# Kernel optimization log

Measured on AMD Instinct MI355X. Metric: run time of the kernel, lower is better.

## Reference

```python
import jax, jax.numpy as jnp
import numpy as np

B, H, W, BLK = 32, 512, 512, 8
QF_MIN, QF_MAX, QF_BIAS = 2.0, 50.0, 0.0

_RGB2YCC = jnp.array([[0.299, 0.587, 0.114],
                      [-0.168736, -0.331264, 0.5],
                      [0.5, -0.418688, -0.081312]], jnp.float32)
_YCC_OFF = jnp.array([0.0, 128.0, 128.0], jnp.float32)

Y_QTB = jnp.array([16,11,10,16,24,40,51,61,12,12,14,19,26,58,60,55,14,13,16,24,40,57,69,56,
                   14,17,22,29,51,87,80,62,18,22,37,56,68,109,103,77,24,36,55,64,81,104,113,92,
                   49,64,78,87,103,121,120,101,72,92,95,98,112,100,103,99], jnp.float32).reshape(8, 8)
C_QTB = jnp.array([17,18,24,47,99,99,99,99,18,21,26,66,99,99,99,99,24,26,56,99,99,99,99,99,
                   47,66,99,99,99,99,99,99,99,99,99,99,99,99,99,99,99,99,99,99,99,99,99,99,
                   99,99,99,99,99,99,99,99,99,99,99,99,99,99,99,99], jnp.float32).reshape(8, 8)

# orthonormal 8x8 DCT-II matrix
_k = np.arange(8.0)[:, None]; _n = np.arange(8.0)[None, :]
_C = 0.5 * np.cos((2 * _n + 1) * _k * np.pi / 16.0)
_C[0] *= 1.0 / np.sqrt(2.0)
DCT_M = jnp.asarray(_C, jnp.float32)

# standard JPEG zig-zag raster order over the 64 coefficients of an 8x8 block
ZIGZAG = jnp.array([0,1,8,16,9,2,3,10,17,24,32,25,18,11,4,5,12,19,26,33,40,48,41,34,27,20,13,6,
                    7,14,21,28,35,42,49,56,57,50,43,36,29,22,15,23,30,37,44,51,58,59,52,45,38,31,
                    39,46,53,60,61,54,47,55,62,63], jnp.int32)


def hard_round(x):
    # straight-through round: forward = round(x), backward = identity
    return x + jax.lax.stop_gradient(jnp.round(x) - x)


def split_blocks(x):
    # [B,H,W] -> [B,H/8,W/8,8,8]
    b, h, w = x.shape
    return x.reshape(b, h // BLK, BLK, w // BLK, BLK).transpose(0, 1, 3, 2, 4)


def dct2d(x):
    # 2D DCT over the trailing 8x8 dims: C @ X @ C^T
    return jnp.einsum('ij,bnmjk,lk->bnmil', DCT_M, x, DCT_M)


def _norm01(e):
    mn = e.min(axis=(1, 2), keepdims=True)
    mx = e.max(axis=(1, 2), keepdims=True)
    return (e - mn) / (mx - mn + 1e-6)


def _ac_energy(d):
    # per-block log AC energy, shape [B,h8,w8]
    return jnp.log1p(jnp.sum(d * d, axis=(-2, -1)) - d[..., 0, 0] ** 2 + 1e-6)


def _forward(rgb):
    ycbcr = hard_round(jnp.einsum('bhwc,kc->bhwk', rgb, _RGB2YCC) + _YCC_OFF) - 128.0
    y_d = dct2d(split_blocks(ycbcr[..., 0]))
    cb_d = dct2d(split_blocks(ycbcr[..., 1]))
    cr_d = dct2d(split_blocks(ycbcr[..., 2]))

    # QFMapGenerator (default): per-block AC-energy rank in [0,1], upsampled to pixels
    rank = jnp.stack([_norm01(_ac_energy(y_d)),
                      _norm01(0.5 * (_ac_energy(cb_d) + _ac_energy(cr_d)))], axis=-1)  # [B,h8,w8,2]
    rank_px = jnp.repeat(jnp.repeat(rank, BLK, axis=1), BLK, axis=2)  # [B,H,W,2]

    # RankToQF
    enc_qf = jnp.clip(hard_round(QF_MIN + rank_px * (QF_MAX - QF_MIN) + QF_BIAS), QF_MIN, QF_MAX)
    y_qf_min = enc_qf[..., 0].min(axis=(1, 2), keepdims=True)
    y_qf_max = enc_qf[..., 0].max(axis=(1, 2), keepdims=True)
    c_qf_min = enc_qf[..., 1].min(axis=(1, 2), keepdims=True)
    c_qf_max = enc_qf[..., 1].max(axis=(1, 2), keepdims=True)

    # QFToScale: standard JPEG QF -> scale factor
    enc_scale = hard_round(jnp.where(enc_qf < 50.0, 5000.0 / enc_qf, 200.0 - 2.0 * enc_qf)) / 100.0

    sy = split_blocks(enc_scale[..., 0])  # [B,h8,w8,8,8]
    sc = split_blocks(enc_scale[..., 1])
    yq = hard_round(y_d / (sy * Y_QTB))
    cbq = hard_round(cb_d / (sc * C_QTB))
    crq = hard_round(cr_d / (sc * C_QTB))
    qdct = jnp.stack([yq, cbq, crq], axis=1)  # [B,3,h8,w8,8,8]

    nb = (H // BLK) * (W // BLK)
    flat = qdct.reshape(B, 3, nb, 64)
    # delta encode along the block axis
    delta = jnp.concatenate([flat[:, :, :1], flat[:, :, 1:] - flat[:, :, :-1]], axis=2)
    # zig-zag raster scan of the 64 coefficients
    zz = delta[..., ZIGZAG]
    blocks = jnp.log(jnp.abs(zz) + 1.0) / jnp.log(2.0)
    blocks = blocks.reshape(-1, 64)
    return qdct, blocks, enc_qf, enc_scale, y_qf_min, y_qf_max, c_qf_min, c_qf_max


def setup_inputs() -> dict:
    key = jax.random.key(0)
    rgb = jax.random.uniform(key, (B, H, W, 3), jnp.float32) * 255.0
    return {"rgb": rgb}


def reference(rgb):
    return _forward(rgb)
```

## Files before the change

### kernel.cpp

```cpp
#include <hip/hip_runtime.h>
#include <math.h>

#define BB 32
#define HH 512
#define WW 512
#define NB 4096
#define QD 25165824
#define PP 16777216
#define TAILOFF (2 * (size_t)QD + 2 * (size_t)PP)

constexpr int ZZc[64] = {
    0,1,8,16,9,2,3,10,17,24,32,25,18,11,4,5,12,19,26,33,40,48,41,34,27,20,13,6,
    7,14,21,28,35,42,49,56,57,50,43,36,29,22,15,23,30,37,44,51,58,59,52,45,38,31,
    39,46,53,60,61,54,47,55,62,63};
__constant__ int c_zz[64] = {
    0,1,8,16,9,2,3,10,17,24,32,25,18,11,4,5,12,19,26,33,40,48,41,34,27,20,13,6,
    7,14,21,28,35,42,49,56,57,50,43,36,29,22,15,23,30,37,44,51,58,59,52,45,38,31,
    39,46,53,60,61,54,47,55,62,63};

struct QArg { float Cf[64]; double rqY[64]; double rqC[64]; };

__device__ __forceinline__ double qf_from_rank(double r) {
    double q = rint(2.0 + r * 48.0 + 0.0);
    return fmin(fmax(q, 2.0), 50.0);
}
__device__ __forceinline__ double scale_from_qf(double qf) {
    double s = (qf < 50.0) ? (5000.0 / qf) : (200.0 - 2.0 * qf);
    return rint(s) / 100.0;
}

__device__ __forceinline__ void ycc16(const float* __restrict__ src, int p0,
                                      int* y, int* cb, int* cr) {
    float px[48];
    const float4* s4 = (const float4*)(src + (size_t)p0 * 3);
    #pragma unroll
    for (int k = 0; k < 12; ++k) ((float4*)px)[k] = s4[k];
    #pragma unroll
    for (int k = 0; k < 16; ++k) {
        double R = px[3 * k], G = px[3 * k + 1], Bv = px[3 * k + 2];
        y[k]  = (int)(rint(R * (double)0.299f     + G * (double)0.587f     + Bv * (double)0.114f)             - 128.0);
        cb[k] = (int)(rint(R * (double)-0.168736f + G * (double)-0.331264f + Bv * (double)0.5f       + 128.0) - 128.0);
        cr[k] = (int)(rint(R * (double)0.5f       + G * (double)-0.418688f + Bv * (double)-0.081312f + 128.0) - 128.0);
    }
}

__global__ __launch_bounds__(256, 4) void k_energy(const float* __restrict__ rgb,
                                                   double* __restrict__ ey,
                                                   double* __restrict__ ec) {
    __shared__ int4 part[3][8][32];
    __shared__ double ecomb[2][64];
    int b = blockIdx.x >> 6, i = blockIdx.x & 63, t = threadIdx.x;
    const float* src = rgb + (size_t)(b * HH + i * 8) * WW * 3;
    {
        int y[16], cb[16], cr[16];
        ycc16(src, t * 16, y, cb, cr);
        int s[3][2] = {{0,0},{0,0},{0,0}}, s2[3][2] = {{0,0},{0,0},{0,0}};
        #pragma unroll
        for (int k = 0; k < 16; ++k) {
            int h = k >> 3;
            s[0][h] += y[k];  s2[0][h] += y[k] * y[k];
            s[1][h] += cb[k]; s2[1][h] += cb[k] * cb[k];
            s[2][h] += cr[k]; s2[2][h] += cr[k] * cr[k];
        }
        int r0 = t >> 5, c = t & 31;
        #pragma unroll
        for (int ch = 0; ch < 3; ++ch)
            part[ch][r0][c] = make_int4(s[ch][0], s2[ch][0], s[ch][1], s2[ch][1]);
    }
    __syncthreads();
    int ch = t >> 6, j = t & 63;
    if (ch < 3) {
        int S = 0, S2 = 0;
        #pragma unroll
        for (int r = 0; r < 8; ++r) {
            const int2* p = (const int2*)&part[ch][r][j >> 1];
            int2 v = p[j & 1];
            S += v.x; S2 += v.y;
        }
        double e = log1p((double)S2 - (double)S * (double)S * (1.0 / 64.0) + 1e-6);
        if (ch == 0) ey[b * NB + i * 64 + j] = e;
        else ecomb[ch - 1][j] = e;
    }
    __syncthreads();
    if (t < 64) ec[b * NB + i * 64 + t] = 0.5 * (ecomb[0][t] + ecomb[1][t]);
}

__global__ __launch_bounds__(256) void k_minmax(const double* __restrict__ ey,
                                                const double* __restrict__ ec,
                                                double* __restrict__ mm,
                                                float* __restrict__ out_tail) {
    __shared__ double s0[256], s1[256], s2[256], s3[256];
    int b = blockIdx.x, tid = threadIdx.x;
    double mny = 1e300, mxy = -1e300, mnc = 1e300, mxc = -1e300;
    for (int n = tid; n < NB; n += 256) {
        double vy = ey[b * NB + n], vc = ec[b * NB + n];
        mny = fmin(mny, vy); mxy = fmax(mxy, vy);
        mnc = fmin(mnc, vc); mxc = fmax(mxc, vc);
    }
    s0[tid] = mny; s1[tid] = mxy; s2[tid] = mnc; s3[tid] = mxc;
    __syncthreads();
    for (int off = 128; off > 0; off >>= 1) {
        if (tid < off) {
            s0[tid] = fmin(s0[tid], s0[tid + off]);
            s1[tid] = fmax(s1[tid], s1[tid + off]);
            s2[tid] = fmin(s2[tid], s2[tid + off]);
            s3[tid] = fmax(s3[tid], s3[tid + off]);
        }
        __syncthreads();
    }
    if (tid == 0) {
        mm[b] = s0[0]; mm[32 + b] = s1[0]; mm[64 + b] = s2[0]; mm[96 + b] = s3[0];
        double ry = (s1[0] - s0[0]) / (s1[0] - s0[0] + 1e-6);
        double rc = (s3[0] - s2[0]) / (s3[0] - s2[0] + 1e-6);
        out_tail[b]      = (float)qf_from_rank(0.0);
        out_tail[32 + b] = (float)qf_from_rank(ry);
        out_tail[64 + b] = (float)qf_from_rank(0.0);
        out_tail[96 + b] = (float)qf_from_rank(rc);
    }
}

__global__ __launch_bounds__(256, 3) void k_quant(const float* __restrict__ rgb,
                                                  QArg A,
                                                  const double* __restrict__ ey,
                                                  const double* __restrict__ ec,
                                                  const double* __restrict__ mm,
                                                  float* __restrict__ out) {
    __shared__ __align__(16) char lds[53248];
    short* sqA = (short*)lds;
    short* sqB = (short*)(lds + 26112);
    float4* qsc = (float4*)(lds + 52224);
    short* planes = (short*)lds;

    int b = blockIdx.x >> 6, i = blockIdx.x & 63, t = threadIdx.x;
    {
        int y[16], cb[16], cr[16];
        ycc16(rgb + (size_t)(b * HH + i * 8) * WW * 3, t * 16, y, cb, cr);
        alignas(16) short yb[16], cbb[16], crb[16];
        #pragma unroll
        for (int k = 0; k < 16; ++k) {
            yb[k] = (short)y[k]; cbb[k] = (short)cb[k]; crb[k] = (short)cr[k];
        }
        int4* d0 = (int4*)&planes[0 * 4096 + 16 * t];
        int4* d1 = (int4*)&planes[1 * 4096 + 16 * t];
        int4* d2 = (int4*)&planes[2 * 4096 + 16 * t];
        d0[0] = ((int4*)yb)[0];  d0[1] = ((int4*)yb)[1];
        d1[0] = ((int4*)cbb)[0]; d1[1] = ((int4*)cbb)[1];
        d2[0] = ((int4*)crb)[0]; d2[1] = ((int4*)crb)[1];
    }
    __syncthreads();
    int ch = t >> 6, j = t & 63;
    float U[8][8];
    double qy = 0, qc = 0, sy = 1, sc = 1;
    if (ch < 3) {
        int gt = b * NB + i * 64 + j;
        double eyv = ey[gt], ecv = ec[gt];
        double mny = mm[b], mxy = mm[32 + b], mnc = mm[64 + b], mxc = mm[96 + b];
        double ry = (eyv - mny) / (mxy - mny + 1e-6);
        double rc = (ecv - mnc) / (mxc - mnc + 1e-6);
        qy = qf_from_rank(ry); qc = qf_from_rank(rc);
        sy = scale_from_qf(qy); sc = scale_from_qf(qc);
        #pragma unroll
        for (int r = 0; r < 8; ++r) {
            alignas(16) short xs[8];
            *(int4*)xs = *(const int4*)&planes[ch * 4096 + r * 512 + j * 8];
            float xr[8];
            #pragma unroll
            for (int s = 0; s < 8; ++s) xr[s] = (float)xs[s];
            #pragma unroll
            for (int v = 0; v < 8; ++v) {
                float u = 0.0f;
                #pragma unroll
                for (int s = 0; s < 8; ++s) u += xr[s] * A.Cf[v * 8 + s];
                U[r][v] = u;
            }
        }
    }
    __syncthreads();
    if (ch < 3) {
        if (ch == 0) qsc[j] = make_float4((float)qy, (float)qc, (float)sy, (float)sc);
        double rinv = 1.0 / ((ch == 0) ? sy : sc);
        const double* rqt = (ch == 0) ? A.rqY : A.rqC;
        int row = (ch * 64 + j) * 68;
        int qp[32];
        #pragma unroll
        for (int u = 0; u < 8; ++u) {
            alignas(8) short srow[8];
            #pragma unroll
            for (int v = 0; v < 8; ++v) {
                float dq = (float)rint([&]{
                    float d = 0.0f;
                    #pragma unroll
                    for (int r = 0; r < 8; ++r) d += A.Cf[u * 8 + r] * U[r][v];
                    return (double)d * (rqt[u * 8 + v] * rinv);
                }());
                srow[v] = (short)(int)dq;
            }
            ((long long*)&sqA[row + u * 8])[0] = ((long long*)srow)[0];
            ((long long*)&sqA[row + u * 8 + 4])[0] = ((long long*)srow)[1];
            #pragma unroll
            for (int h = 0; h < 4; ++h)
                qp[u * 4 + h] = ((int)srow[2 * h] & 0xffff) |
                                ((int)((unsigned)(int)srow[2 * h + 1] << 16));
        }
        int pp[32];
        #pragma unroll
        for (int w = 0; w < 32; ++w) pp[w] = __shfl_up(qp[w], 1, 64);
        #pragma unroll
        for (int g = 0; g < 8; ++g) {
            alignas(8) short dz[8];
            #pragma unroll
            for (int e = 0; e < 8; ++e) {
                int m = ZZc[g * 8 + e];
                int w = m >> 1;
                int cu = (m & 1) ? (qp[w] >> 16) : ((qp[w] << 16) >> 16);
                int pv = (m & 1) ? (pp[w] >> 16) : ((pp[w] << 16) >> 16);
                dz[e] = (short)(cu - pv);
            }
            ((long long*)&sqB[row + g * 8])[0] = ((long long*)dz)[0];
            ((long long*)&sqB[row + g * 8 + 4])[0] = ((long long*)dz)[1];
        }
    }
    __syncthreads();

    size_t obase = ((size_t)b * 3 * NB + (size_t)i * 64) * 64;
    #pragma unroll
    for (int it = 0; it < 12; ++it) {
        int m = it * 256 + t;
        int mch = m >> 10, f = m & 1023;
        int mj = f >> 4, k4 = (f & 15) * 4;
        alignas(8) short s4[4];
        *(long long*)s4 = *(const long long*)&sqA[(mch * 64 + mj) * 68 + k4];
        float4 v = make_float4((float)s4[0], (float)s4[1], (float)s4[2], (float)s4[3]);
        *(float4*)(out + obase + (size_t)mch * NB * 64 + (size_t)mj * 64 + k4) = v;
    }
    #pragma unroll
    for (int it = 0; it < 12; ++it) {
        int m = it * 256 + t;
        int mch = m >> 10, f = m & 1023;
        int mj = f >> 4, k4 = (f & 15) * 4;
        alignas(8) short d4[4];
        *(long long*)d4 = *(const long long*)&sqB[(mch * 64 + mj) * 68 + k4];
        float4 v = make_float4(log2f(fabsf((float)d4[0]) + 1.0f),
                               log2f(fabsf((float)d4[1]) + 1.0f),
                               log2f(fabsf((float)d4[2]) + 1.0f),
                               log2f(fabsf((float)d4[3]) + 1.0f));
        *(float4*)(out + QD + obase + (size_t)mch * NB * 64 + (size_t)mj * 64 + k4) = v;
    }
    {
        float4 qs = qsc[t >> 2];
        float4 qv = make_float4(qs.x, qs.y, qs.x, qs.y);
        float4 sv = make_float4(qs.z, qs.w, qs.z, qs.w);
        float2* mq = (float2*)(out + 2 * (size_t)QD);
        float2* ms = (float2*)(out + 2 * (size_t)QD + PP);
        #pragma unroll
        for (int rr = 0; rr < 8; ++rr) {
            size_t P = ((size_t)(b * HH + i * 8 + rr)) * WW;
            ((float4*)(mq + P))[t] = qv;
            ((float4*)(ms + P))[t] = sv;
        }
    }
}

__global__ __launch_bounds__(256) void k_fix(const float* __restrict__ q,
                                             float* __restrict__ ob) {
    int idx = blockIdx.x * 256 + threadIdx.x;
    int rid = idx >> 6, k = idx & 63;
    int bch = rid >> 6;
    int i = rid & 63;
    size_t base = ((size_t)bch * NB + (size_t)i * 64) * 64;
    int zk = c_zz[k];
    float cur = q[base + zk];
    float prv = (i > 0) ? q[base - 64 + zk] : 0.0f;
    ob[base + k] = log2f(fabsf(cur - prv) + 1.0f);
}

extern "C" void kernel_launch(void* const* d_in, const int* in_sizes, int n_in,
                              void* d_out, int out_size, void* d_ws, size_t ws_size,
                              hipStream_t stream) {
    const float* rgb = (const float*)d_in[0];
    float* out = (float*)d_out;
    double* ws = (double*)d_ws;
    double* ey = ws;
    double* ec = ws + (size_t)BB * NB;
    double* mm = ws + 2 * (size_t)BB * NB;

    static const double YQ[64] = {
        16,11,10,16,24,40,51,61, 12,12,14,19,26,58,60,55, 14,13,16,24,40,57,69,56,
        14,17,22,29,51,87,80,62, 18,22,37,56,68,109,103,77, 24,36,55,64,81,104,113,92,
        49,64,78,87,103,121,120,101, 72,92,95,98,112,100,103,99};
    static const double CQ[64] = {
        17,18,24,47,99,99,99,99, 18,21,26,66,99,99,99,99, 24,26,56,99,99,99,99,99,
        47,66,99,99,99,99,99,99, 99,99,99,99,99,99,99,99, 99,99,99,99,99,99,99,99,
        99,99,99,99,99,99,99,99, 99,99,99,99,99,99,99,99};

    QArg qa;
    for (int k = 0; k < 8; ++k)
        for (int n = 0; n < 8; ++n) {
            double v = 0.5 * cos((2.0 * n + 1.0) * (double)k * M_PI / 16.0);
            if (k == 0) v *= 0.70710678118654752440;
            qa.Cf[k * 8 + n] = (float)v;
        }
    for (int k = 0; k < 64; ++k) { qa.rqY[k] = 1.0 / YQ[k]; qa.rqC[k] = 1.0 / CQ[k]; }

    dim3 blk(256);
    k_energy<<<BB * 64, blk, 0, stream>>>(rgb, ey, ec);
    k_minmax<<<BB, blk, 0, stream>>>(ey, ec, mm, out + TAILOFF);
    k_quant<<<BB * 64, blk, 0, stream>>>(rgb, qa, ey, ec, mm, out);
    k_fix<<<(BB * 3 * 64 * 64) / 256, blk, 0, stream>>>(out, out + QD);
}
```

Before: 430.7 us.

## Cache YCbCr planes as int16 in workspace and compute delta-zigzag from LDS

k_energy now writes the rounded YCbCr values as int16 planes to workspace, and k_quant reads them back instead of reloading the float RGB input and redoing the colour conversion. The delta/zigzag stage no longer packs values and uses cross-lane shuffles into a second LDS buffer. It reads the quantized coefficients of the current and previous block straight from sqA. Dropping the rgb reload (about 3x fewer bytes) and the second LDS buffer shrinks LDS, so occupancy is raised to 4 blocks per CU. The cost is an extra global int16 write and read of about 50 MB per call.

```diff
diff --git a/kernel.cpp b/kernel.cpp
--- a/kernel.cpp
+++ b/kernel.cpp
@@ -9,10 +9,6 @@
 #define PP 16777216
 #define TAILOFF (2 * (size_t)QD + 2 * (size_t)PP)
 
-constexpr int ZZc[64] = {
-    0,1,8,16,9,2,3,10,17,24,32,25,18,11,4,5,12,19,26,33,40,48,41,34,27,20,13,6,
-    7,14,21,28,35,42,49,56,57,50,43,36,29,22,15,23,30,37,44,51,58,59,52,45,38,31,
-    39,46,53,60,61,54,47,55,62,63};
 __constant__ int c_zz[64] = {
     0,1,8,16,9,2,3,10,17,24,32,25,18,11,4,5,12,19,26,33,40,48,41,34,27,20,13,6,
     7,14,21,28,35,42,49,56,57,50,43,36,29,22,15,23,30,37,44,51,58,59,52,45,38,31,
@@ -45,6 +41,7 @@
 }
 
 __global__ __launch_bounds__(256, 4) void k_energy(const float* __restrict__ rgb,
+                                                   short* __restrict__ planes,
                                                    double* __restrict__ ey,
                                                    double* __restrict__ ec) {
     __shared__ int4 part[3][8][32];
@@ -55,13 +52,22 @@
         int y[16], cb[16], cr[16];
         ycc16(src, t * 16, y, cb, cr);
         int s[3][2] = {{0,0},{0,0},{0,0}}, s2[3][2] = {{0,0},{0,0},{0,0}};
+        alignas(16) short yb[16], cbb[16], crb[16];
         #pragma unroll
         for (int k = 0; k < 16; ++k) {
             int h = k >> 3;
             s[0][h] += y[k];  s2[0][h] += y[k] * y[k];
             s[1][h] += cb[k]; s2[1][h] += cb[k] * cb[k];
             s[2][h] += cr[k]; s2[2][h] += cr[k] * cr[k];
-        }
+            yb[k] = (short)y[k]; cbb[k] = (short)cb[k]; crb[k] = (short)cr[k];
+        }
+        size_t soff = (size_t)i * 4096 + (size_t)t * 16;
+        short* d0 = planes + (((size_t)(b * 3 + 0)) << 18) + soff;
+        short* d1 = planes + (((size_t)(b * 3 + 1)) << 18) + soff;
+        short* d2 = planes + (((size_t)(b * 3 + 2)) << 18) + soff;
+        ((int4*)d0)[0] = ((int4*)yb)[0];  ((int4*)d0)[1] = ((int4*)yb)[1];
+        ((int4*)d1)[0] = ((int4*)cbb)[0]; ((int4*)d1)[1] = ((int4*)cbb)[1];
+        ((int4*)d2)[0] = ((int4*)crb)[0]; ((int4*)d2)[1] = ((int4*)crb)[1];
         int r0 = t >> 5, c = t & 31;
         #pragma unroll
         for (int ch = 0; ch < 3; ++ch)
@@ -119,35 +125,17 @@
     }
 }
 
-__global__ __launch_bounds__(256, 3) void k_quant(const float* __restrict__ rgb,
+__global__ __launch_bounds__(256, 4) void k_quant(const short* __restrict__ planes,
                                                   QArg A,
                                                   const double* __restrict__ ey,
                                                   const double* __restrict__ ec,
                                                   const double* __restrict__ mm,
                                                   float* __restrict__ out) {
-    __shared__ __align__(16) char lds[53248];
+    __shared__ __align__(16) char lds[27136];
     short* sqA = (short*)lds;
-    short* sqB = (short*)(lds + 26112);
-    float4* qsc = (float4*)(lds + 52224);
-    short* planes = (short*)lds;
+    float4* qsc = (float4*)(lds + 26112);
 
     int b = blockIdx.x >> 6, i = blockIdx.x & 63, t = threadIdx.x;
-    {
-        int y[16], cb[16], cr[16];
-        ycc16(rgb + (size_t)(b * HH + i * 8) * WW * 3, t * 16, y, cb, cr);
-        alignas(16) short yb[16], cbb[16], crb[16];
-        #pragma unroll
-        for (int k = 0; k < 16; ++k) {
-            yb[k] = (short)y[k]; cbb[k] = (short)cb[k]; crb[k] = (short)cr[k];
-        }
-        int4* d0 = (int4*)&planes[0 * 4096 + 16 * t];
-        int4* d1 = (int4*)&planes[1 * 4096 + 16 * t];
-        int4* d2 = (int4*)&planes[2 * 4096 + 16 * t];
-        d0[0] = ((int4*)yb)[0];  d0[1] = ((int4*)yb)[1];
-        d1[0] = ((int4*)cbb)[0]; d1[1] = ((int4*)cbb)[1];
-        d2[0] = ((int4*)crb)[0]; d2[1] = ((int4*)crb)[1];
-    }
-    __syncthreads();
     int ch = t >> 6, j = t & 63;
     float U[8][8];
     double qy = 0, qc = 0, sy = 1, sc = 1;
@@ -159,10 +147,12 @@
         double rc = (ecv - mnc) / (mxc - mnc + 1e-6);
         qy = qf_from_rank(ry); qc = qf_from_rank(rc);
         sy = scale_from_qf(qy); sc = scale_from_qf(qc);
+        const short* pl = planes + (((size_t)(b * 3 + ch)) << 18)
+                        + (size_t)i * 4096 + (size_t)j * 8;
         #pragma unroll
         for (int r = 0; r < 8; ++r) {
             alignas(16) short xs[8];
-            *(int4*)xs = *(const int4*)&planes[ch * 4096 + r * 512 + j * 8];
+            *(int4*)xs = *(const int4*)(pl + (size_t)r * 512);
             float xr[8];
             #pragma unroll
             for (int s = 0; s < 8; ++s) xr[s] = (float)xs[s];
@@ -174,14 +164,10 @@
                 U[r][v] = u;
             }
         }
-    }
-    __syncthreads();
-    if (ch < 3) {
         if (ch == 0) qsc[j] = make_float4((float)qy, (float)qc, (float)sy, (float)sc);
         double rinv = 1.0 / ((ch == 0) ? sy : sc);
         const double* rqt = (ch == 0) ? A.rqY : A.rqC;
         int row = (ch * 64 + j) * 68;
-        int qp[32];
         #pragma unroll
         for (int u = 0; u < 8; ++u) {
             alignas(8) short srow[8];
@@ -197,53 +183,38 @@
             }
             ((long long*)&sqA[row + u * 8])[0] = ((long long*)srow)[0];
             ((long long*)&sqA[row + u * 8 + 4])[0] = ((long long*)srow)[1];
-            #pragma unroll
-            for (int h = 0; h < 4; ++h)
-                qp[u * 4 + h] = ((int)srow[2 * h] & 0xffff) |
-                                ((int)((unsigned)(int)srow[2 * h + 1] << 16));
-        }
-        int pp[32];
-        #pragma unroll
-        for (int w = 0; w < 32; ++w) pp[w] = __shfl_up(qp[w], 1, 64);
-        #pragma unroll
-        for (int g = 0; g < 8; ++g) {
-            alignas(8) short dz[8];
-            #pragma unroll
-            for (int e = 0; e < 8; ++e) {
-                int m = ZZc[g * 8 + e];
-                int w = m >> 1;
-                int cu = (m & 1) ? (qp[w] >> 16) : ((qp[w] << 16) >> 16);
-                int pv = (m & 1) ? (pp[w] >> 16) : ((pp[w] << 16) >> 16);
-                dz[e] = (short)(cu - pv);
-            }
-            ((long long*)&sqB[row + g * 8])[0] = ((long long*)dz)[0];
-            ((long long*)&sqB[row + g * 8 + 4])[0] = ((long long*)dz)[1];
         }
     }
     __syncthreads();
 
     size_t obase = ((size_t)b * 3 * NB + (size_t)i * 64) * 64;
+    int k4 = (t & 15) * 4;
     #pragma unroll
     for (int it = 0; it < 12; ++it) {
         int m = it * 256 + t;
         int mch = m >> 10, f = m & 1023;
-        int mj = f >> 4, k4 = (f & 15) * 4;
+        int mj = f >> 4;
         alignas(8) short s4[4];
         *(long long*)s4 = *(const long long*)&sqA[(mch * 64 + mj) * 68 + k4];
         float4 v = make_float4((float)s4[0], (float)s4[1], (float)s4[2], (float)s4[3]);
         *(float4*)(out + obase + (size_t)mch * NB * 64 + (size_t)mj * 64 + k4) = v;
     }
+    int zk0 = c_zz[k4], zk1 = c_zz[k4 + 1], zk2 = c_zz[k4 + 2], zk3 = c_zz[k4 + 3];
     #pragma unroll
     for (int it = 0; it < 12; ++it) {
         int m = it * 256 + t;
         int mch = m >> 10, f = m & 1023;
-        int mj = f >> 4, k4 = (f & 15) * 4;
-        alignas(8) short d4[4];
-        *(long long*)d4 = *(const long long*)&sqB[(mch * 64 + mj) * 68 + k4];
-        float4 v = make_float4(log2f(fabsf((float)d4[0]) + 1.0f),
-                               log2f(fabsf((float)d4[1]) + 1.0f),
-                               log2f(fabsf((float)d4[2]) + 1.0f),
-                               log2f(fabsf((float)d4[3]) + 1.0f));
+        int mj = f >> 4;
+        int rowc = (mch * 64 + mj) * 68;
+        int rowp = rowc - (mj ? 68 : 0);
+        float d0 = (float)(sqA[rowc + zk0] - sqA[rowp + zk0]);
+        float d1 = (float)(sqA[rowc + zk1] - sqA[rowp + zk1]);
+        float d2 = (float)(sqA[rowc + zk2] - sqA[rowp + zk2]);
+        float d3 = (float)(sqA[rowc + zk3] - sqA[rowp + zk3]);
+        float4 v = make_float4(log2f(fabsf(d0) + 1.0f),
+                               log2f(fabsf(d1) + 1.0f),
+                               log2f(fabsf(d2) + 1.0f),
+                               log2f(fabsf(d3) + 1.0f));
         *(float4*)(out + QD + obase + (size_t)mch * NB * 64 + (size_t)mj * 64 + k4) = v;
     }
     {
@@ -283,6 +254,7 @@
     double* ey = ws;
     double* ec = ws + (size_t)BB * NB;
     double* mm = ws + 2 * (size_t)BB * NB;
+    short* planes = (short*)(ws + 2 * (size_t)BB * NB + 128);
 
     static const double YQ[64] = {
         16,11,10,16,24,40,51,61, 12,12,14,19,26,58,60,55, 14,13,16,24,40,57,69,56,
@@ -303,8 +275,8 @@
     for (int k = 0; k < 64; ++k) { qa.rqY[k] = 1.0 / YQ[k]; qa.rqC[k] = 1.0 / CQ[k]; }
 
     dim3 blk(256);
-    k_energy<<<BB * 64, blk, 0, stream>>>(rgb, ey, ec);
+    k_energy<<<BB * 64, blk, 0, stream>>>(rgb, planes, ey, ec);
     k_minmax<<<BB, blk, 0, stream>>>(ey, ec, mm, out + TAILOFF);
-    k_quant<<<BB * 64, blk, 0, stream>>>(rgb, qa, ey, ec, mm, out);
+    k_quant<<<BB * 64, blk, 0, stream>>>(planes, qa, ey, ec, mm, out);
     k_fix<<<(BB * 3 * 64 * 64) / 256, blk, 0, stream>>>(out, out + QD);
 }
```

After: 435.3 us. No clear change (+1.1%).
